# Kernel tuning notes

Hardware: AMD Instinct MI355X
Metric: run time of the kernel (lower is better)

Reference implementation:

```python
import jax, jax.numpy as jnp
import numpy as np

BZ, QL, KL, D = 8, 2048, 2048, 128
SCALE = 1.0 / (D ** 0.5)
NEG = -1000000000.0


def setup_inputs() -> dict:
    key = jax.random.key(0)
    kq, kk, kv, km = jax.random.split(key, 4)
    q = jax.random.normal(kq, (BZ, QL, D), dtype=jnp.float32)
    k = jax.random.normal(kk, (BZ, KL, D), dtype=jnp.float32)
    v = jax.random.normal(kv, (BZ, KL, D), dtype=jnp.float32)
    mask = jax.random.randint(km, (BZ, KL), 0, 2).astype(jnp.bool_)
    return {"q": q, "k": k, "v": v, "mask": mask}


def reference(q, k, v, mask):
    # scores: (bz, q_len, k_len)
    score = jnp.einsum('bqd,bkd->bqk', q, k) * SCALE
    # masked_fill where ~mask (padding positions) with -1e9
    score = jnp.where(mask[:, None, :], score, NEG)
    weights = jax.nn.softmax(score, axis=-1)
    # (bz, q_len, v_dim)
    return jnp.einsum('bqk,bkd->bqd', weights, v)
```

## Files before the change

### kernel.cpp

```cpp
#include <hip/hip_runtime.h>
#include <hip/hip_bf16.h>


#define BZ 8
#define QL 2048
#define KLEN 2048
#define DH 128
#define NSL 64
#define SLICE_E 4096
#define PPITCH 40

typedef float f32x4 __attribute__((ext_vector_type(4)));
typedef int   i32x4 __attribute__((ext_vector_type(4)));
typedef __bf16 bf16x8 __attribute__((ext_vector_type(8)));
typedef __bf16 bf16x4 __attribute__((ext_vector_type(4)));
typedef __bf16 bf16x2 __attribute__((ext_vector_type(2)));

#define QSC 0.12751879523298232f
#define NEGV -1000000000.0f

__global__ void prep_kv(const float* __restrict__ kg, const float* __restrict__ vg,
                        __bf16* __restrict__ khat, __bf16* __restrict__ vhat) {
  const int blk = blockIdx.x;
  const int bs = blk & 511;
  const int b = bs >> 6, s = bs & 63;
  const int tid = threadIdx.x;
#pragma unroll
  for (int i = 0; i < 2; ++i) {
    const int c = i * 256 + tid;
    const int ln = c & 63, lc = ln & 15, qd = ln >> 4;
    if (blk < 512) {
      const int ff = (c >> 6) & 1, kf = c >> 7;
      const int key = s * 32 + ff * 16 + lc;
      const float* src = kg + ((size_t)(b * KLEN + key)) * DH + kf * 32 + qd * 8;
      f32x4 a = *(const f32x4*)src;
      f32x4 d = *(const f32x4*)(src + 4);
      bf16x8 w;
      w[0]=(__bf16)a[0]; w[1]=(__bf16)a[1]; w[2]=(__bf16)a[2]; w[3]=(__bf16)a[3];
      w[4]=(__bf16)d[0]; w[5]=(__bf16)d[1]; w[6]=(__bf16)d[2]; w[7]=(__bf16)d[3];
      *(bf16x8*)&khat[((size_t)bs * 512 + c) * 8] = w;
    } else {
      const int nt = c >> 6;
      const float* src = vg + ((size_t)(b * KLEN + s * 32 + qd * 8)) * DH + nt * 16 + lc;
      bf16x8 w;
#pragma unroll
      for (int j = 0; j < 8; ++j) w[j] = (__bf16)src[(size_t)j * DH];
      *(bf16x8*)&vhat[((size_t)bs * 512 + c) * 8] = w;
    }
  }
}

__global__ __launch_bounds__(512, 2) void fattn8(
    const __bf16* __restrict__ khat, const __bf16* __restrict__ vhat,
    const float* __restrict__ qg_, const int* __restrict__ maskg,
    float* __restrict__ outg) {
  __shared__ __align__(16) __bf16 sP[8][2][16 * PPITCH];
  __shared__ __align__(16) float fb[8192 + 64];

  const int tid = threadIdx.x;
  const int wv = tid >> 6, ln = tid & 63;
  const int qd = ln >> 4, lc = ln & 15;
  const int ab = blockIdx.x & 7, qt = blockIdx.x >> 3;
  const int q0 = qt * 64;
  const int qg = wv & 1, sl = wv >> 1;

  bf16x8 qf[2][4];
#pragma unroll
  for (int qp = 0; qp < 2; ++qp) {
    const float* qr = qg_ + ((size_t)(ab * QL + q0 + qg * 32 + qp * 16 + lc)) * DH + qd * 8;
#pragma unroll
    for (int kf = 0; kf < 4; ++kf) {
      f32x4 a = *(const f32x4*)(qr + kf * 32);
      f32x4 c = *(const f32x4*)(qr + kf * 32 + 4);
      bf16x8 t;
      t[0]=(__bf16)(a[0]*QSC); t[1]=(__bf16)(a[1]*QSC); t[2]=(__bf16)(a[2]*QSC); t[3]=(__bf16)(a[3]*QSC);
      t[4]=(__bf16)(c[0]*QSC); t[5]=(__bf16)(c[1]*QSC); t[6]=(__bf16)(c[2]*QSC); t[7]=(__bf16)(c[3]*QSC);
      qf[qp][kf] = t;
    }
  }

  const __bf16* Kb = khat + (size_t)ab * NSL * SLICE_E;
  const __bf16* Vb = vhat + (size_t)ab * NSL * SLICE_E;
  const int* mrow = maskg + ab * KLEN;
  __bf16* sp0 = &sP[wv][0][0];
  __bf16* sp1 = &sP[wv][1][0];

  f32x4 oacc[2][8];
#pragma unroll
  for (int qp = 0; qp < 2; ++qp)
#pragma unroll
    for (int i = 0; i < 8; ++i) oacc[qp][i] = (f32x4){0.f, 0.f, 0.f, 0.f};
  float li[2] = {0.f, 0.f};

  bf16x8 kA[4][2], kB[4][2], vA[8];
  bf16x8 pf0, pf1;
  i32x4 mA0, mA1, mB0, mB1;
  f32x4 sa[2][2];
  const int s0 = sl * 16;

  auto loadK = [&](bf16x8 (&dst)[4][2], int sidx) {
    const __bf16* ks = Kb + (size_t)sidx * SLICE_E;
#pragma unroll
    for (int kf = 0; kf < 4; ++kf)
#pragma unroll
      for (int f = 0; f < 2; ++f)
        dst[kf][f] = *(const bf16x8*)&ks[((kf * 2 + f) * 64 + ln) * 8];
  };
  auto loadM = [&](i32x4& m0, i32x4& m1, int sidx) {
    m0 = *(const i32x4*)&mrow[sidx * 32 + qd * 4];
    m1 = *(const i32x4*)&mrow[sidx * 32 + 16 + qd * 4];
  };
  auto loadV = [&](int sidx) {
    const __bf16* vs = Vb + (size_t)sidx * SLICE_E;
#pragma unroll
    for (int nt = 0; nt < 8; ++nt)
      vA[nt] = *(const bf16x8*)&vs[(nt * 64 + ln) * 8];
  };
  auto qk = [&](const bf16x8 (&kk)[4][2]) {
#pragma unroll
    for (int f = 0; f < 2; ++f)
#pragma unroll
      for (int qp = 0; qp < 2; ++qp) sa[f][qp] = (f32x4){0.f, 0.f, 0.f, 0.f};
#pragma unroll
    for (int kf = 0; kf < 4; ++kf)
#pragma unroll
      for (int f = 0; f < 2; ++f) {
        sa[f][0] = __builtin_amdgcn_mfma_f32_16x16x32_bf16(kk[kf][f], qf[0][kf], sa[f][0], 0, 0, 0);
        sa[f][1] = __builtin_amdgcn_mfma_f32_16x16x32_bf16(kk[kf][f], qf[1][kf], sa[f][1], 0, 0, 0);
      }
  };
  auto pv = [&]() {
#pragma unroll
    for (int nt = 0; nt < 8; ++nt) {
      oacc[0][nt] = __builtin_amdgcn_mfma_f32_16x16x32_bf16(vA[nt], pf0, oacc[0][nt], 0, 0, 0);
      oacc[1][nt] = __builtin_amdgcn_mfma_f32_16x16x32_bf16(vA[nt], pf1, oacc[1][nt], 0, 0, 0);
    }
  };
  auto softmax = [&](const i32x4& m0, const i32x4& m1) {
#pragma unroll
    for (int qp = 0; qp < 2; ++qp) {
      float ps[2][4];
#pragma unroll
      for (int r = 0; r < 4; ++r) {
        float p0 = __builtin_amdgcn_exp2f(sa[0][qp][r]);
        float p1 = __builtin_amdgcn_exp2f(sa[1][qp][r]);
        ps[0][r] = m0[r] ? p0 : 0.f;
        ps[1][r] = m1[r] ? p1 : 0.f;
      }
      li[qp] += ((ps[0][0] + ps[0][1]) + (ps[0][2] + ps[0][3])) +
                ((ps[1][0] + ps[1][1]) + (ps[1][2] + ps[1][3]));
      __bf16* sp = (qp == 0) ? sp0 : sp1;
#pragma unroll
      for (int f = 0; f < 2; ++f) {
        bf16x4 pw;
        pw[0] = (__bf16)ps[f][0]; pw[1] = (__bf16)ps[f][1];
        pw[2] = (__bf16)ps[f][2]; pw[3] = (__bf16)ps[f][3];
        *(bf16x4*)&sp[lc * PPITCH + f * 16 + qd * 4] = pw;
      }
    }
    pf0 = *(const bf16x8*)&sp0[lc * PPITCH + qd * 8];
    pf1 = *(const bf16x8*)&sp1[lc * PPITCH + qd * 8];
  };

  loadK(kA, s0);
  loadM(mA0, mA1, s0);
  loadK(kB, s0 + 1);
  loadM(mB0, mB1, s0 + 1);
  loadV(s0);
  qk(kA);
  softmax(mA0, mA1);

  for (int du = 0; du < 7; ++du) {
    {
      const int it = 2 * du + 1, s = s0 + it;
      loadK(kA, s + 1);
      loadM(mA0, mA1, s + 1);
      qk(kB);
      pv();
      loadV(s);
      softmax(mB0, mB1);
    }
    {
      const int it = 2 * du + 2, s = s0 + it;
      loadK(kB, s + 1);
      loadM(mB0, mB1, s + 1);
      qk(kA);
      pv();
      loadV(s);
      softmax(mA0, mA1);
    }
  }
  {
    const int s = s0 + 15;
    qk(kB);
    pv();
    loadV(s);
    softmax(mB0, mB1);
  }
  pv();

#pragma unroll
  for (int qp = 0; qp < 2; ++qp) {
    li[qp] += __shfl_xor(li[qp], 16, 64);
    li[qp] += __shfl_xor(li[qp], 32, 64);
  }

  f32x4* mOv = (f32x4*)fb;
  float* sml = fb + 8192;
  auto publish = [&]() {
#pragma unroll
    for (int qp = 0; qp < 2; ++qp) {
#pragma unroll
      for (int nt = 0; nt < 8; ++nt)
        mOv[((qg * 2 + qp) * 8 + nt) * 64 + ln] = oacc[qp][nt];
      if (qd == 0) sml[(qg * 2 + qp) * 16 + lc] = li[qp];
    }
  };
  auto absorb = [&]() {
#pragma unroll
    for (int qp = 0; qp < 2; ++qp) {
      li[qp] += sml[(qg * 2 + qp) * 16 + lc];
#pragma unroll
      for (int nt = 0; nt < 8; ++nt) {
        f32x4 o2 = mOv[((qg * 2 + qp) * 8 + nt) * 64 + ln];
#pragma unroll
        for (int r = 0; r < 4; ++r) oacc[qp][nt][r] += o2[r];
      }
    }
  };

  __syncthreads();
  if (sl == 3) publish();
  __syncthreads();
  if (sl == 2) absorb();
  __syncthreads();
  if (sl == 1) publish();
  __syncthreads();
  if (sl == 0) absorb();
  __syncthreads();
  if (sl == 2) publish();
  __syncthreads();
  if (sl == 0) {
    absorb();
#pragma unroll
    for (int qp = 0; qp < 2; ++qp) {
      const float invL = 1.0f / li[qp];
      float* orow = outg + ((size_t)(ab * QL + q0 + qg * 32 + qp * 16 + lc)) * DH;
#pragma unroll
      for (int nt = 0; nt < 8; ++nt) {
        f32x4 res;
#pragma unroll
        for (int r = 0; r < 4; ++r) res[r] = oacc[qp][nt][r] * invL;
        *(f32x4*)&orow[nt * 16 + qd * 4] = res;
      }
    }
  }
}

#define KT 64
#define KPITCH 136
#define VPITCH 72
#define PPITCH2 72

__global__ __launch_bounds__(256, 1) void fattn_mono(
    const float* __restrict__ qgp, const float* __restrict__ kg,
    const float* __restrict__ vg, const int* __restrict__ maskg,
    float* __restrict__ outg) {
  __shared__ __bf16 sK[KT][KPITCH];
  __shared__ __bf16 sVT[DH][VPITCH];
  __shared__ __bf16 sPm[4][16][PPITCH2];

  const int tid = threadIdx.x;
  const int wv = tid >> 6, ln = tid & 63;
  const int qd = ln >> 4, lc = ln & 15;
  const int bid = blockIdx.x;
  const int b = bid >> 5;
  const int q0 = (bid & 31) << 6;
  const int qw = q0 + (wv << 4);

  bf16x8 qf[4];
  {
    const float* qr = qgp + ((size_t)(b * QL + qw + lc)) * DH + qd * 8;
#pragma unroll
    for (int kf = 0; kf < 4; ++kf) {
      f32x4 a = *(const f32x4*)(qr + kf * 32);
      f32x4 c = *(const f32x4*)(qr + kf * 32 + 4);
      bf16x8 t;
      t[0]=(__bf16)(a[0]*QSC); t[1]=(__bf16)(a[1]*QSC); t[2]=(__bf16)(a[2]*QSC); t[3]=(__bf16)(a[3]*QSC);
      t[4]=(__bf16)(c[0]*QSC); t[5]=(__bf16)(c[1]*QSC); t[6]=(__bf16)(c[2]*QSC); t[7]=(__bf16)(c[3]*QSC);
      qf[kf] = t;
    }
  }

  const float* kb = kg + (size_t)b * KLEN * DH;
  const float* vb = vg + (size_t)b * KLEN * DH;
  const int* mrow = maskg + b * KLEN;

  f32x4 kreg[8], va[4], vbr[4];

  auto load_tile = [&](int t) {
    const float* kt = kb + ((size_t)t * KT) * DH;
#pragma unroll
    for (int it = 0; it < 8; ++it) {
      int f = it * 256 + tid;
      kreg[it] = *(const f32x4*)(kt + (size_t)(f >> 5) * DH + (f & 31) * 4);
    }
    const float* vt = vb + ((size_t)t * KT) * DH;
#pragma unroll
    for (int it = 0; it < 4; ++it) {
      int u = it * 256 + tid;
      int m = u & 31, dc = (u >> 5) * 4;
      va[it]  = *(const f32x4*)(vt + (size_t)(2 * m) * DH + dc);
      vbr[it] = *(const f32x4*)(vt + (size_t)(2 * m + 1) * DH + dc);
    }
  };
  auto store_tile = [&]() {
#pragma unroll
    for (int it = 0; it < 8; ++it) {
      int f = it * 256 + tid;
      bf16x4 w;
      w[0]=(__bf16)kreg[it][0]; w[1]=(__bf16)kreg[it][1];
      w[2]=(__bf16)kreg[it][2]; w[3]=(__bf16)kreg[it][3];
      *(bf16x4*)&sK[f >> 5][(f & 31) * 4] = w;
    }
#pragma unroll
    for (int it = 0; it < 4; ++it) {
      int u = it * 256 + tid;
      int m = u & 31, dc = (u >> 5) * 4;
#pragma unroll
      for (int j = 0; j < 4; ++j) {
        bf16x2 p2;
        p2[0] = (__bf16)va[it][j];
        p2[1] = (__bf16)vbr[it][j];
        *(bf16x2*)&sVT[dc + j][2 * m] = p2;
      }
    }
  };

  f32x4 oacc[8];
#pragma unroll
  for (int i = 0; i < 8; ++i) oacc[i] = (f32x4){0.f, 0.f, 0.f, 0.f};
  float mi[4] = {-INFINITY, -INFINITY, -INFINITY, -INFINITY};
  float li[4] = {0.f, 0.f, 0.f, 0.f};

  load_tile(0); store_tile(); __syncthreads();

  for (int t = 0; t < (KLEN / KT); ++t) {
    const bool more = (t + 1 < (KLEN / KT));
    if (more) load_tile(t + 1);

    f32x4 sa[4];
#pragma unroll
    for (int f = 0; f < 4; ++f) sa[f] = (f32x4){0.f, 0.f, 0.f, 0.f};
#pragma unroll
    for (int kf = 0; kf < 4; ++kf)
#pragma unroll
      for (int f = 0; f < 4; ++f) {
        bf16x8 bk = *(const bf16x8*)&sK[f * 16 + lc][kf * 32 + qd * 8];
        sa[f] = __builtin_amdgcn_mfma_f32_16x16x32_bf16(qf[kf], bk, sa[f], 0, 0, 0);
      }

    const int kv0 = t * KT;
#pragma unroll
    for (int f = 0; f < 4; ++f) {
      const bool keep = mrow[kv0 + f * 16 + lc] != 0;
#pragma unroll
      for (int r = 0; r < 4; ++r) sa[f][r] = keep ? sa[f][r] : NEGV;
    }

    float rm[4], alpha[4], rs[4];
#pragma unroll
    for (int r = 0; r < 4; ++r)
      rm[r] = fmaxf(fmaxf(sa[0][r], sa[1][r]), fmaxf(sa[2][r], sa[3][r]));
#pragma unroll
    for (int sh = 0; sh < 4; ++sh) {
      const int off = 1 << sh;
#pragma unroll
      for (int r = 0; r < 4; ++r) rm[r] = fmaxf(rm[r], __shfl_xor(rm[r], off, 64));
    }
#pragma unroll
    for (int r = 0; r < 4; ++r) {
      float mn = fmaxf(mi[r], rm[r]);
      alpha[r] = __builtin_amdgcn_exp2f(mi[r] - mn);
      mi[r] = mn; rs[r] = 0.f;
    }
#pragma unroll
    for (int f = 0; f < 4; ++f)
#pragma unroll
      for (int r = 0; r < 4; ++r) {
        float p = __builtin_amdgcn_exp2f(sa[f][r] - mi[r]);
        sa[f][r] = p; rs[r] += p;
      }
#pragma unroll
    for (int sh = 0; sh < 4; ++sh) {
      const int off = 1 << sh;
#pragma unroll
      for (int r = 0; r < 4; ++r) rs[r] += __shfl_xor(rs[r], off, 64);
    }
#pragma unroll
    for (int r = 0; r < 4; ++r) li[r] = li[r] * alpha[r] + rs[r];

#pragma unroll
    for (int f = 0; f < 4; ++f)
#pragma unroll
      for (int r = 0; r < 4; ++r)
        sPm[wv][qd * 4 + r][f * 16 + lc] = (__bf16)sa[f][r];
#pragma unroll
    for (int nt = 0; nt < 8; ++nt)
#pragma unroll
      for (int r = 0; r < 4; ++r) oacc[nt][r] *= alpha[r];

#pragma unroll
    for (int kp = 0; kp < 2; ++kp) {
      bf16x8 ap = *(const bf16x8*)&sPm[wv][lc][kp * 32 + qd * 8];
#pragma unroll
      for (int nt = 0; nt < 8; ++nt) {
        bf16x8 bv = *(const bf16x8*)&sVT[nt * 16 + lc][kp * 32 + qd * 8];
        oacc[nt] = __builtin_amdgcn_mfma_f32_16x16x32_bf16(ap, bv, oacc[nt], 0, 0, 0);
      }
    }

    __syncthreads();
    if (more) store_tile();
    __syncthreads();
  }

  float inv[4];
#pragma unroll
  for (int r = 0; r < 4; ++r) inv[r] = 1.0f / li[r];
  float* orow = outg + ((size_t)(b * QL + qw)) * DH;
#pragma unroll
  for (int nt = 0; nt < 8; ++nt)
#pragma unroll
    for (int r = 0; r < 4; ++r)
      orow[(size_t)(qd * 4 + r) * DH + nt * 16 + lc] = oacc[nt][r] * inv[r];
}

extern "C" void kernel_launch(void* const* d_in, const int* in_sizes, int n_in,
                              void* d_out, int out_size, void* d_ws, size_t ws_size,
                              hipStream_t stream) {
  (void)in_sizes; (void)n_in; (void)out_size;
  const float* q = (const float*)d_in[0];
  const float* k = (const float*)d_in[1];
  const float* v = (const float*)d_in[2];
  const int* mask = (const int*)d_in[3];
  float* out = (float*)d_out;

  const size_t kv_elems = (size_t)BZ * KLEN * DH;
  if (ws_size >= 2 * kv_elems * sizeof(__bf16)) {
    __bf16* khat = (__bf16*)d_ws;
    __bf16* vhat = khat + kv_elems;
    prep_kv<<<dim3(1024), dim3(256), 0, stream>>>(k, v, khat, vhat);
    fattn8<<<dim3(256), dim3(512), 0, stream>>>(khat, vhat, q, mask, out);
  } else {
    fattn_mono<<<dim3(BZ * (QL / 64)), dim3(256), 0, stream>>>(q, k, v, mask, out);
  }
}
```

Measured before the change: 104.6 us.

## Stage K/V slices through LDS with async global-to-LDS loads and double buffering

Replaces direct global-to-register K/V loads with global_load_lds DMA into double-buffered shared-memory slots. The two query-group waves sharing a key slice each fetch half of it. Per-iteration __syncthreads and MFMA s_setprio hints are added, and prep_kv's block-to-(batch,slice) mapping is reordered so consecutive blocks touch different batches. The aim is to halve redundant global traffic across the paired waves and hide load latency, at the cost of more LDS use (which may reduce occupancy) and block-wide barriers every iteration.

```diff
diff --git a/kernel.cpp b/kernel.cpp
--- a/kernel.cpp
+++ b/kernel.cpp
@@ -19,11 +19,17 @@
 #define QSC 0.12751879523298232f
 #define NEGV -1000000000.0f
 
+__device__ __forceinline__ void gload_lds16(const __bf16* g, __bf16* l) {
+  __builtin_amdgcn_global_load_lds(
+      (const __attribute__((address_space(1))) void*)g,
+      (__attribute__((address_space(3))) void*)l, 16, 0, 0);
+}
+
 __global__ void prep_kv(const float* __restrict__ kg, const float* __restrict__ vg,
                         __bf16* __restrict__ khat, __bf16* __restrict__ vhat) {
   const int blk = blockIdx.x;
   const int bs = blk & 511;
-  const int b = bs >> 6, s = bs & 63;
+  const int b = bs & 7, s = bs >> 3;
   const int tid = threadIdx.x;
 #pragma unroll
   for (int i = 0; i < 2; ++i) {
@@ -38,24 +44,25 @@
       bf16x8 w;
       w[0]=(__bf16)a[0]; w[1]=(__bf16)a[1]; w[2]=(__bf16)a[2]; w[3]=(__bf16)a[3];
       w[4]=(__bf16)d[0]; w[5]=(__bf16)d[1]; w[6]=(__bf16)d[2]; w[7]=(__bf16)d[3];
-      *(bf16x8*)&khat[((size_t)bs * 512 + c) * 8] = w;
+      *(bf16x8*)&khat[((size_t)(b * 64 + s) * 512 + c) * 8] = w;
     } else {
       const int nt = c >> 6;
       const float* src = vg + ((size_t)(b * KLEN + s * 32 + qd * 8)) * DH + nt * 16 + lc;
       bf16x8 w;
 #pragma unroll
       for (int j = 0; j < 8; ++j) w[j] = (__bf16)src[(size_t)j * DH];
-      *(bf16x8*)&vhat[((size_t)bs * 512 + c) * 8] = w;
+      *(bf16x8*)&vhat[((size_t)(b * 64 + s) * 512 + c) * 8] = w;
     }
   }
 }
 
-__global__ __launch_bounds__(512, 2) void fattn8(
+__global__ __launch_bounds__(512, 2) void fattn9(
     const __bf16* __restrict__ khat, const __bf16* __restrict__ vhat,
     const float* __restrict__ qg_, const int* __restrict__ maskg,
     float* __restrict__ outg) {
+  __shared__ __align__(16) __bf16 kst[2][4][SLICE_E];
+  __shared__ __align__(16) __bf16 vst[2][4][SLICE_E];
   __shared__ __align__(16) __bf16 sP[8][2][16 * PPITCH];
-  __shared__ __align__(16) float fb[8192 + 64];
 
   const int tid = threadIdx.x;
   const int wv = tid >> 6, ln = tid & 63;
@@ -92,31 +99,42 @@
     for (int i = 0; i < 8; ++i) oacc[qp][i] = (f32x4){0.f, 0.f, 0.f, 0.f};
   float li[2] = {0.f, 0.f};
 
-  bf16x8 kA[4][2], kB[4][2], vA[8];
+  bf16x8 kReg[4][2], vReg[8];
   bf16x8 pf0, pf1;
   i32x4 mA0, mA1, mB0, mB1;
   f32x4 sa[2][2];
   const int s0 = sl * 16;
 
-  auto loadK = [&](bf16x8 (&dst)[4][2], int sidx) {
-    const __bf16* ks = Kb + (size_t)sidx * SLICE_E;
-#pragma unroll
-    for (int kf = 0; kf < 4; ++kf)
-#pragma unroll
-      for (int f = 0; f < 2; ++f)
-        dst[kf][f] = *(const bf16x8*)&ks[((kf * 2 + f) * 64 + ln) * 8];
+  auto stage = [&](int slot, int sidx) {
+    const __bf16* ks = Kb + (size_t)sidx * SLICE_E + qg * 2048;
+    const __bf16* vs = Vb + (size_t)sidx * SLICE_E + qg * 2048;
+    __bf16* kd = &kst[slot][sl][qg * 2048];
+    __bf16* vd = &vst[slot][sl][qg * 2048];
+#pragma unroll
+    for (int i = 0; i < 4; ++i) {
+      gload_lds16(ks + (i * 64 + ln) * 8, kd + i * 512);
+      gload_lds16(vs + (i * 64 + ln) * 8, vd + i * 512);
+    }
   };
   auto loadM = [&](i32x4& m0, i32x4& m1, int sidx) {
     m0 = *(const i32x4*)&mrow[sidx * 32 + qd * 4];
     m1 = *(const i32x4*)&mrow[sidx * 32 + 16 + qd * 4];
   };
-  auto loadV = [&](int sidx) {
-    const __bf16* vs = Vb + (size_t)sidx * SLICE_E;
+  auto readK = [&](int slot) {
+    const __bf16* kb = &kst[slot][sl][0];
+#pragma unroll
+    for (int kf = 0; kf < 4; ++kf)
+#pragma unroll
+      for (int f = 0; f < 2; ++f)
+        kReg[kf][f] = *(const bf16x8*)&kb[((kf * 2 + f) * 64 + ln) * 8];
+  };
+  auto readV = [&](int slot) {
+    const __bf16* vb2 = &vst[slot][sl][0];
 #pragma unroll
     for (int nt = 0; nt < 8; ++nt)
-      vA[nt] = *(const bf16x8*)&vs[(nt * 64 + ln) * 8];
-  };
-  auto qk = [&](const bf16x8 (&kk)[4][2]) {
+      vReg[nt] = *(const bf16x8*)&vb2[(nt * 64 + ln) * 8];
+  };
+  auto qk = [&]() {
 #pragma unroll
     for (int f = 0; f < 2; ++f)
 #pragma unroll
@@ -125,15 +143,15 @@
     for (int kf = 0; kf < 4; ++kf)
 #pragma unroll
       for (int f = 0; f < 2; ++f) {
-        sa[f][0] = __builtin_amdgcn_mfma_f32_16x16x32_bf16(kk[kf][f], qf[0][kf], sa[f][0], 0, 0, 0);
-        sa[f][1] = __builtin_amdgcn_mfma_f32_16x16x32_bf16(kk[kf][f], qf[1][kf], sa[f][1], 0, 0, 0);
+        sa[f][0] = __builtin_amdgcn_mfma_f32_16x16x32_bf16(kReg[kf][f], qf[0][kf], sa[f][0], 0, 0, 0);
+        sa[f][1] = __builtin_amdgcn_mfma_f32_16x16x32_bf16(kReg[kf][f], qf[1][kf], sa[f][1], 0, 0, 0);
       }
   };
   auto pv = [&]() {
 #pragma unroll
     for (int nt = 0; nt < 8; ++nt) {
-      oacc[0][nt] = __builtin_amdgcn_mfma_f32_16x16x32_bf16(vA[nt], pf0, oacc[0][nt], 0, 0, 0);
-      oacc[1][nt] = __builtin_amdgcn_mfma_f32_16x16x32_bf16(vA[nt], pf1, oacc[1][nt], 0, 0, 0);
+      oacc[0][nt] = __builtin_amdgcn_mfma_f32_16x16x32_bf16(vReg[nt], pf0, oacc[0][nt], 0, 0, 0);
+      oacc[1][nt] = __builtin_amdgcn_mfma_f32_16x16x32_bf16(vReg[nt], pf1, oacc[1][nt], 0, 0, 0);
     }
   };
   auto softmax = [&](const i32x4& m0, const i32x4& m1) {
@@ -162,39 +180,55 @@
     pf1 = *(const bf16x8*)&sp1[lc * PPITCH + qd * 8];
   };
 
-  loadK(kA, s0);
+  stage(0, s0);
   loadM(mA0, mA1, s0);
-  loadK(kB, s0 + 1);
   loadM(mB0, mB1, s0 + 1);
-  loadV(s0);
-  qk(kA);
+  __syncthreads();
+
+  stage(1, s0 + 1);
+  readK(0);
+  __builtin_amdgcn_s_setprio(1);
+  qk();
+  __builtin_amdgcn_s_setprio(0);
+  readV(0);
   softmax(mA0, mA1);
+  __syncthreads();
 
   for (int du = 0; du < 7; ++du) {
     {
-      const int it = 2 * du + 1, s = s0 + it;
-      loadK(kA, s + 1);
+      const int s = s0 + 2 * du + 1;
+      stage(0, s + 1);
       loadM(mA0, mA1, s + 1);
-      qk(kB);
+      readK(1);
+      __builtin_amdgcn_s_setprio(1);
+      qk();
       pv();
-      loadV(s);
+      __builtin_amdgcn_s_setprio(0);
+      readV(1);
       softmax(mB0, mB1);
+      __syncthreads();
     }
     {
-      const int it = 2 * du + 2, s = s0 + it;
-      loadK(kB, s + 1);
+      const int s = s0 + 2 * du + 2;
+      stage(1, s + 1);
       loadM(mB0, mB1, s + 1);
-      qk(kA);
+      readK(0);
+      __builtin_amdgcn_s_setprio(1);
+      qk();
       pv();
-      loadV(s);
+      __builtin_amdgcn_s_setprio(0);
+      readV(0);
       softmax(mA0, mA1);
+      __syncthreads();
     }
   }
   {
-    const int s = s0 + 15;
-    qk(kB);
+    readK(1);
+    __builtin_amdgcn_s_setprio(1);
+    qk();
     pv();
-    loadV(s);
+    __builtin_amdgcn_s_setprio(0);
+    readV(1);
     softmax(mB0, mB1);
   }
   pv();
@@ -205,6 +239,7 @@
     li[qp] += __shfl_xor(li[qp], 32, 64);
   }
 
+  float* fb = (float*)&kst[0][0][0];
   f32x4* mOv = (f32x4*)fb;
   float* sml = fb + 8192;
   auto publish = [&]() {
@@ -451,7 +486,7 @@
     __bf16* khat = (__bf16*)d_ws;
     __bf16* vhat = khat + kv_elems;
     prep_kv<<<dim3(1024), dim3(256), 0, stream>>>(k, v, khat, vhat);
-    fattn8<<<dim3(256), dim3(512), 0, stream>>>(khat, vhat, q, mask, out);
+    fattn9<<<dim3(256), dim3(512), 0, stream>>>(khat, vhat, q, mask, out);
   } else {
     fattn_mono<<<dim3(BZ * (QL / 64)), dim3(256), 0, stream>>>(q, k, v, mask, out);
   }
```

New measurement: 107.7 us. +2.9%, slower.

## Double-buffer V fragments, add per-iteration barrier and MFMA priority boost

Applied to the files above, without the earlier changes.

V fragments are now double-buffered (vA/vB), so the next slice's V loads are issued ahead of the QK and PV MFMAs rather than after them. This hides global load latency behind matrix work. Each iteration also adds a workgroup barrier to keep waves in step and raises wave priority around the MFMA block. The prep kernel now interleaves batches across block indices, which changes the order in which blocks write K/V but not the layout. Costs are more VGPRs at 2 blocks per CU and barrier stalls every slice.

```diff
diff --git a/kernel.cpp b/kernel.cpp
--- a/kernel.cpp
+++ b/kernel.cpp
@@ -23,7 +23,7 @@
                         __bf16* __restrict__ khat, __bf16* __restrict__ vhat) {
   const int blk = blockIdx.x;
   const int bs = blk & 511;
-  const int b = bs >> 6, s = bs & 63;
+  const int b = bs & 7, s = bs >> 3;
   const int tid = threadIdx.x;
 #pragma unroll
   for (int i = 0; i < 2; ++i) {
@@ -38,19 +38,19 @@
       bf16x8 w;
       w[0]=(__bf16)a[0]; w[1]=(__bf16)a[1]; w[2]=(__bf16)a[2]; w[3]=(__bf16)a[3];
       w[4]=(__bf16)d[0]; w[5]=(__bf16)d[1]; w[6]=(__bf16)d[2]; w[7]=(__bf16)d[3];
-      *(bf16x8*)&khat[((size_t)bs * 512 + c) * 8] = w;
+      *(bf16x8*)&khat[((size_t)(b * 64 + s) * 512 + c) * 8] = w;
     } else {
       const int nt = c >> 6;
       const float* src = vg + ((size_t)(b * KLEN + s * 32 + qd * 8)) * DH + nt * 16 + lc;
       bf16x8 w;
 #pragma unroll
       for (int j = 0; j < 8; ++j) w[j] = (__bf16)src[(size_t)j * DH];
-      *(bf16x8*)&vhat[((size_t)bs * 512 + c) * 8] = w;
+      *(bf16x8*)&vhat[((size_t)(b * 64 + s) * 512 + c) * 8] = w;
     }
   }
 }
 
-__global__ __launch_bounds__(512, 2) void fattn8(
+__global__ __launch_bounds__(512, 2) void fattn10(
     const __bf16* __restrict__ khat, const __bf16* __restrict__ vhat,
     const float* __restrict__ qg_, const int* __restrict__ maskg,
     float* __restrict__ outg) {
@@ -92,7 +92,7 @@
     for (int i = 0; i < 8; ++i) oacc[qp][i] = (f32x4){0.f, 0.f, 0.f, 0.f};
   float li[2] = {0.f, 0.f};
 
-  bf16x8 kA[4][2], kB[4][2], vA[8];
+  bf16x8 kA[4][2], kB[4][2], vA[8], vB[8];
   bf16x8 pf0, pf1;
   i32x4 mA0, mA1, mB0, mB1;
   f32x4 sa[2][2];
@@ -106,16 +106,16 @@
       for (int f = 0; f < 2; ++f)
         dst[kf][f] = *(const bf16x8*)&ks[((kf * 2 + f) * 64 + ln) * 8];
   };
+  auto loadV = [&](bf16x8 (&dst)[8], int sidx) {
+    const __bf16* vs = Vb + (size_t)sidx * SLICE_E;
+#pragma unroll
+    for (int nt = 0; nt < 8; ++nt)
+      dst[nt] = *(const bf16x8*)&vs[(nt * 64 + ln) * 8];
+  };
   auto loadM = [&](i32x4& m0, i32x4& m1, int sidx) {
     m0 = *(const i32x4*)&mrow[sidx * 32 + qd * 4];
     m1 = *(const i32x4*)&mrow[sidx * 32 + 16 + qd * 4];
   };
-  auto loadV = [&](int sidx) {
-    const __bf16* vs = Vb + (size_t)sidx * SLICE_E;
-#pragma unroll
-    for (int nt = 0; nt < 8; ++nt)
-      vA[nt] = *(const bf16x8*)&vs[(nt * 64 + ln) * 8];
-  };
   auto qk = [&](const bf16x8 (&kk)[4][2]) {
 #pragma unroll
     for (int f = 0; f < 2; ++f)
@@ -129,11 +129,11 @@
         sa[f][1] = __builtin_amdgcn_mfma_f32_16x16x32_bf16(kk[kf][f], qf[1][kf], sa[f][1], 0, 0, 0);
       }
   };
-  auto pv = [&]() {
+  auto pv = [&](const bf16x8 (&vv)[8]) {
 #pragma unroll
     for (int nt = 0; nt < 8; ++nt) {
-      oacc[0][nt] = __builtin_amdgcn_mfma_f32_16x16x32_bf16(vA[nt], pf0, oacc[0][nt], 0, 0, 0);
-      oacc[1][nt] = __builtin_amdgcn_mfma_f32_16x16x32_bf16(vA[nt], pf1, oacc[1][nt], 0, 0, 0);
+      oacc[0][nt] = __builtin_amdgcn_mfma_f32_16x16x32_bf16(vv[nt], pf0, oacc[0][nt], 0, 0, 0);
+      oacc[1][nt] = __builtin_amdgcn_mfma_f32_16x16x32_bf16(vv[nt], pf1, oacc[1][nt], 0, 0, 0);
     }
   };
   auto softmax = [&](const i32x4& m0, const i32x4& m1) {
@@ -166,38 +166,47 @@
   loadM(mA0, mA1, s0);
   loadK(kB, s0 + 1);
   loadM(mB0, mB1, s0 + 1);
-  loadV(s0);
+  loadV(vA, s0);
   qk(kA);
   softmax(mA0, mA1);
 
   for (int du = 0; du < 7; ++du) {
     {
-      const int it = 2 * du + 1, s = s0 + it;
+      const int s = s0 + 2 * du + 1;
+      __builtin_amdgcn_s_barrier();
       loadK(kA, s + 1);
+      loadV(vB, s);
       loadM(mA0, mA1, s + 1);
+      __builtin_amdgcn_s_setprio(1);
       qk(kB);
-      pv();
-      loadV(s);
+      pv(vA);
+      __builtin_amdgcn_s_setprio(0);
       softmax(mB0, mB1);
     }
     {
-      const int it = 2 * du + 2, s = s0 + it;
+      const int s = s0 + 2 * du + 2;
+      __builtin_amdgcn_s_barrier();
       loadK(kB, s + 1);
+      loadV(vA, s);
       loadM(mB0, mB1, s + 1);
+      __builtin_amdgcn_s_setprio(1);
       qk(kA);
-      pv();
-      loadV(s);
+      pv(vB);
+      __builtin_amdgcn_s_setprio(0);
       softmax(mA0, mA1);
     }
   }
   {
     const int s = s0 + 15;
+    __builtin_amdgcn_s_barrier();
+    loadV(vB, s);
+    __builtin_amdgcn_s_setprio(1);
     qk(kB);
-    pv();
-    loadV(s);
+    pv(vA);
+    __builtin_amdgcn_s_setprio(0);
     softmax(mB0, mB1);
   }
-  pv();
+  pv(vB);
 
 #pragma unroll
   for (int qp = 0; qp < 2; ++qp) {
@@ -451,7 +460,7 @@
     __bf16* khat = (__bf16*)d_ws;
     __bf16* vhat = khat + kv_elems;
     prep_kv<<<dim3(1024), dim3(256), 0, stream>>>(k, v, khat, vhat);
-    fattn8<<<dim3(256), dim3(512), 0, stream>>>(khat, vhat, q, mask, out);
+    fattn10<<<dim3(256), dim3(512), 0, stream>>>(khat, vhat, q, mask, out);
   } else {
     fattn_mono<<<dim3(BZ * (QL / 64)), dim3(256), 0, stream>>>(q, k, v, mask, out);
   }
```

Result: slower. 140.8 us (+34.6%).

## Split key range across eight waves per 32-query block and raise MFMA priority

Applied to the files above, without the earlier changes.

The attention kernel now gives each block 32 queries instead of 64. All eight waves split the key dimension, eight slices each, instead of two query groups times four key splits. The grid doubles to 512 blocks, and partial results are merged with a deeper publish/absorb tree that uses two LDS slots. MFMA sections are wrapped in s_setprio to favour matrix work over loads, and prep_kv's block-to-(batch, slice) mapping is interleaved. This trades more reduction barriers and more Q and K/V traffic per query for better occupancy across CUs.

```diff
diff --git a/kernel.cpp b/kernel.cpp
--- a/kernel.cpp
+++ b/kernel.cpp
@@ -23,7 +23,7 @@
                         __bf16* __restrict__ khat, __bf16* __restrict__ vhat) {
   const int blk = blockIdx.x;
   const int bs = blk & 511;
-  const int b = bs >> 6, s = bs & 63;
+  const int b = bs & 7, s = bs >> 3;
   const int tid = threadIdx.x;
 #pragma unroll
   for (int i = 0; i < 2; ++i) {
@@ -38,19 +38,19 @@
       bf16x8 w;
       w[0]=(__bf16)a[0]; w[1]=(__bf16)a[1]; w[2]=(__bf16)a[2]; w[3]=(__bf16)a[3];
       w[4]=(__bf16)d[0]; w[5]=(__bf16)d[1]; w[6]=(__bf16)d[2]; w[7]=(__bf16)d[3];
-      *(bf16x8*)&khat[((size_t)bs * 512 + c) * 8] = w;
+      *(bf16x8*)&khat[((size_t)(b * 64 + s) * 512 + c) * 8] = w;
     } else {
       const int nt = c >> 6;
       const float* src = vg + ((size_t)(b * KLEN + s * 32 + qd * 8)) * DH + nt * 16 + lc;
       bf16x8 w;
 #pragma unroll
       for (int j = 0; j < 8; ++j) w[j] = (__bf16)src[(size_t)j * DH];
-      *(bf16x8*)&vhat[((size_t)bs * 512 + c) * 8] = w;
+      *(bf16x8*)&vhat[((size_t)(b * 64 + s) * 512 + c) * 8] = w;
     }
   }
 }
 
-__global__ __launch_bounds__(512, 2) void fattn8(
+__global__ __launch_bounds__(512, 2) void fattn11(
     const __bf16* __restrict__ khat, const __bf16* __restrict__ vhat,
     const float* __restrict__ qg_, const int* __restrict__ maskg,
     float* __restrict__ outg) {
@@ -61,13 +61,13 @@
   const int wv = tid >> 6, ln = tid & 63;
   const int qd = ln >> 4, lc = ln & 15;
   const int ab = blockIdx.x & 7, qt = blockIdx.x >> 3;
-  const int q0 = qt * 64;
-  const int qg = wv & 1, sl = wv >> 1;
+  const int q0 = qt * 32;
+  const int sl = wv;
 
   bf16x8 qf[2][4];
 #pragma unroll
   for (int qp = 0; qp < 2; ++qp) {
-    const float* qr = qg_ + ((size_t)(ab * QL + q0 + qg * 32 + qp * 16 + lc)) * DH + qd * 8;
+    const float* qr = qg_ + ((size_t)(ab * QL + q0 + qp * 16 + lc)) * DH + qd * 8;
 #pragma unroll
     for (int kf = 0; kf < 4; ++kf) {
       f32x4 a = *(const f32x4*)(qr + kf * 32);
@@ -96,7 +96,7 @@
   bf16x8 pf0, pf1;
   i32x4 mA0, mA1, mB0, mB1;
   f32x4 sa[2][2];
-  const int s0 = sl * 16;
+  const int s0 = sl * 8;
 
   auto loadK = [&](bf16x8 (&dst)[4][2], int sidx) {
     const __bf16* ks = Kb + (size_t)sidx * SLICE_E;
@@ -105,16 +105,16 @@
 #pragma unroll
       for (int f = 0; f < 2; ++f)
         dst[kf][f] = *(const bf16x8*)&ks[((kf * 2 + f) * 64 + ln) * 8];
+  };
+  auto loadV = [&](int sidx) {
+    const __bf16* vs = Vb + (size_t)sidx * SLICE_E;
+#pragma unroll
+    for (int nt = 0; nt < 8; ++nt)
+      vA[nt] = *(const bf16x8*)&vs[(nt * 64 + ln) * 8];
   };
   auto loadM = [&](i32x4& m0, i32x4& m1, int sidx) {
     m0 = *(const i32x4*)&mrow[sidx * 32 + qd * 4];
     m1 = *(const i32x4*)&mrow[sidx * 32 + 16 + qd * 4];
-  };
-  auto loadV = [&](int sidx) {
-    const __bf16* vs = Vb + (size_t)sidx * SLICE_E;
-#pragma unroll
-    for (int nt = 0; nt < 8; ++nt)
-      vA[nt] = *(const bf16x8*)&vs[(nt * 64 + ln) * 8];
   };
   auto qk = [&](const bf16x8 (&kk)[4][2]) {
 #pragma unroll
@@ -170,30 +170,36 @@
   qk(kA);
   softmax(mA0, mA1);
 
-  for (int du = 0; du < 7; ++du) {
+  for (int du = 0; du < 3; ++du) {
     {
-      const int it = 2 * du + 1, s = s0 + it;
+      const int s = s0 + 2 * du + 1;
       loadK(kA, s + 1);
       loadM(mA0, mA1, s + 1);
+      __builtin_amdgcn_s_setprio(1);
       qk(kB);
       pv();
+      __builtin_amdgcn_s_setprio(0);
       loadV(s);
       softmax(mB0, mB1);
     }
     {
-      const int it = 2 * du + 2, s = s0 + it;
+      const int s = s0 + 2 * du + 2;
       loadK(kB, s + 1);
       loadM(mB0, mB1, s + 1);
+      __builtin_amdgcn_s_setprio(1);
       qk(kA);
       pv();
+      __builtin_amdgcn_s_setprio(0);
       loadV(s);
       softmax(mA0, mA1);
     }
   }
   {
-    const int s = s0 + 15;
+    const int s = s0 + 7;
+    __builtin_amdgcn_s_setprio(1);
     qk(kB);
     pv();
+    __builtin_amdgcn_s_setprio(0);
     loadV(s);
     softmax(mB0, mB1);
   }
@@ -207,22 +213,22 @@
 
   f32x4* mOv = (f32x4*)fb;
   float* sml = fb + 8192;
-  auto publish = [&]() {
+  auto publish = [&](int slot) {
 #pragma unroll
     for (int qp = 0; qp < 2; ++qp) {
 #pragma unroll
       for (int nt = 0; nt < 8; ++nt)
-        mOv[((qg * 2 + qp) * 8 + nt) * 64 + ln] = oacc[qp][nt];
-      if (qd == 0) sml[(qg * 2 + qp) * 16 + lc] = li[qp];
-    }
-  };
-  auto absorb = [&]() {
+        mOv[((slot * 2 + qp) * 8 + nt) * 64 + ln] = oacc[qp][nt];
+      if (qd == 0) sml[(slot * 2 + qp) * 16 + lc] = li[qp];
+    }
+  };
+  auto absorb = [&](int slot) {
 #pragma unroll
     for (int qp = 0; qp < 2; ++qp) {
-      li[qp] += sml[(qg * 2 + qp) * 16 + lc];
+      li[qp] += sml[(slot * 2 + qp) * 16 + lc];
 #pragma unroll
       for (int nt = 0; nt < 8; ++nt) {
-        f32x4 o2 = mOv[((qg * 2 + qp) * 8 + nt) * 64 + ln];
+        f32x4 o2 = mOv[((slot * 2 + qp) * 8 + nt) * 64 + ln];
 #pragma unroll
         for (int r = 0; r < 4; ++r) oacc[qp][nt][r] += o2[r];
       }
@@ -230,22 +236,26 @@
   };
 
   __syncthreads();
-  if (sl == 3) publish();
-  __syncthreads();
-  if (sl == 2) absorb();
-  __syncthreads();
-  if (sl == 1) publish();
-  __syncthreads();
-  if (sl == 0) absorb();
-  __syncthreads();
-  if (sl == 2) publish();
+  if (sl == 1) publish(0); else if (sl == 3) publish(1);
+  __syncthreads();
+  if (sl == 0) absorb(0); else if (sl == 2) absorb(1);
+  __syncthreads();
+  if (sl == 5) publish(0); else if (sl == 7) publish(1);
+  __syncthreads();
+  if (sl == 4) absorb(0); else if (sl == 6) absorb(1);
+  __syncthreads();
+  if (sl == 2) publish(0); else if (sl == 6) publish(1);
+  __syncthreads();
+  if (sl == 0) absorb(0); else if (sl == 4) absorb(1);
+  __syncthreads();
+  if (sl == 4) publish(0);
   __syncthreads();
   if (sl == 0) {
-    absorb();
+    absorb(0);
 #pragma unroll
     for (int qp = 0; qp < 2; ++qp) {
       const float invL = 1.0f / li[qp];
-      float* orow = outg + ((size_t)(ab * QL + q0 + qg * 32 + qp * 16 + lc)) * DH;
+      float* orow = outg + ((size_t)(ab * QL + q0 + qp * 16 + lc)) * DH;
 #pragma unroll
       for (int nt = 0; nt < 8; ++nt) {
         f32x4 res;
@@ -451,7 +461,7 @@
     __bf16* khat = (__bf16*)d_ws;
     __bf16* vhat = khat + kv_elems;
     prep_kv<<<dim3(1024), dim3(256), 0, stream>>>(k, v, khat, vhat);
-    fattn8<<<dim3(256), dim3(512), 0, stream>>>(khat, vhat, q, mask, out);
+    fattn11<<<dim3(512), dim3(512), 0, stream>>>(khat, vhat, q, mask, out);
   } else {
     fattn_mono<<<dim3(BZ * (QL / 64)), dim3(256), 0, stream>>>(q, k, v, mask, out);
   }
```

New measurement: 112.8 us. 1.08x slower.
